# Optimization experiments

Hardware: AMD Instinct MI355X
Metric: run time of the kernel (lower is better)

## Reference

```python
import jax, jax.numpy as jnp
import numpy as np

DIM = 1024
B, TI, TJ = 8, 2048, 2048
EPS = 1e-5


def layernorm(x, g, b):
    mu = jnp.mean(x, axis=-1, keepdims=True)
    var = jnp.var(x, axis=-1, keepdims=True)
    return (x - mu) * jax.lax.rsqrt(var + EPS) * g + b


def setup_inputs() -> dict:
    key = jax.random.key(0)
    ks = jax.random.split(key, 12)
    s = 1.0 / np.sqrt(DIM)
    return {
        "target": jax.random.normal(ks[0], (B, TI, DIM), jnp.float32),
        "source_k": jax.random.normal(ks[1], (B, TJ, DIM), jnp.float32),
        "source_v": jax.random.normal(ks[2], (B, TJ, DIM), jnp.float32),
        "Wq": jax.random.uniform(ks[3], (DIM, DIM), jnp.float32, -s, s),
        "bq": jax.random.uniform(ks[4], (DIM,), jnp.float32, -s, s),
        "Wk": jax.random.uniform(ks[5], (DIM, DIM), jnp.float32, -s, s),
        "bk": jax.random.uniform(ks[6], (DIM,), jnp.float32, -s, s),
        "Wv": jax.random.uniform(ks[7], (DIM, DIM), jnp.float32, -s, s),
        "bv": jax.random.uniform(ks[8], (DIM,), jnp.float32, -s, s),
        "g_t": jnp.ones((DIM,), jnp.float32),
        "b_t": jnp.zeros((DIM,), jnp.float32),
        "g_k": jnp.ones((DIM,), jnp.float32),
        "b_k": jnp.zeros((DIM,), jnp.float32),
        "g_v": jnp.ones((DIM,), jnp.float32),
        "b_v": jnp.zeros((DIM,), jnp.float32),
    }


def reference(target, source_k, source_v, Wq, bq, Wk, bk, Wv, bv,
              g_t, b_t, g_k, b_k, g_v, b_v):
    scale = DIM ** (-0.5)
    t = layernorm(target, g_t, b_t)
    sk = layernorm(source_k, g_k, b_k)
    sv = layernorm(source_v, g_v, b_v)
    # torch Linear: x @ W.T + b
    q = jnp.einsum('bid,ed->bie', t, Wq) + bq
    k = jnp.einsum('bjd,ed->bje', sk, Wk) + bk
    v = jnp.einsum('bjd,ed->bje', sv, Wv) + bv
    dots = jnp.einsum('bid,bjd->bij', q, k) * scale
    attn = jax.nn.softmax(dots, axis=2)
    return jnp.einsum('bij,bjd->bid', attn, v)
```

## Files before the change

### kernel.cpp

```cpp
#include <hip/hip_runtime.h>
#include <cstdint>

using u16 = unsigned short;
using u32 = unsigned int;
typedef __attribute__((ext_vector_type(8))) short short8;
typedef __attribute__((ext_vector_type(4))) float f32x4;

__device__ __forceinline__ float bf2f(u16 u) { return __uint_as_float(((u32)u) << 16); }
__device__ __forceinline__ u16 f2bf(float f) {
    u32 u = __float_as_uint(f);
    u32 r = u + 0x7fffu + ((u >> 16) & 1u);
    return (u16)(r >> 16);
}

__device__ __forceinline__ void load_lds16(const void* g, void* l) {
    __builtin_amdgcn_global_load_lds((const __attribute__((address_space(1))) void*)g,
                                     (__attribute__((address_space(3))) void*)l, 16, 0, 0);
}

__device__ __forceinline__ void ln_row(const float* __restrict__ x,
                                       const float* __restrict__ gw,
                                       const float* __restrict__ bw,
                                       u16* __restrict__ y, int row) {
    const int tid = threadIdx.x;
    const float4 v = ((const float4*)(x + (size_t)row * 1024))[tid];
    float s  = v.x + v.y + v.z + v.w;
    float ss = v.x * v.x + v.y * v.y + v.z * v.z + v.w * v.w;
#pragma unroll
    for (int off = 32; off; off >>= 1) {
        s  += __shfl_xor(s, off);
        ss += __shfl_xor(ss, off);
    }
    __shared__ float sm[8];
    const int lane = tid & 63, wid = tid >> 6;
    if (lane == 0) { sm[wid] = s; sm[wid + 4] = ss; }
    __syncthreads();
    s  = sm[0] + sm[1] + sm[2] + sm[3];
    ss = sm[4] + sm[5] + sm[6] + sm[7];
    const float mu   = s * (1.0f / 1024.0f);
    const float var  = ss * (1.0f / 1024.0f) - mu * mu;
    const float rstd = rsqrtf(var + 1e-5f);
    const float4 g4 = ((const float4*)gw)[tid];
    const float4 b4 = ((const float4*)bw)[tid];
    u16 o[4];
    o[0] = f2bf((v.x - mu) * rstd * g4.x + b4.x);
    o[1] = f2bf((v.y - mu) * rstd * g4.y + b4.y);
    o[2] = f2bf((v.z - mu) * rstd * g4.z + b4.z);
    o[3] = f2bf((v.w - mu) * rstd * g4.w + b4.w);
    *(uint2*)(y + (size_t)row * 1024 + tid * 4) = *(uint2*)o;
}

__global__ __launch_bounds__(256)
void ln_cast_kernel(const float* __restrict__ x, const float* __restrict__ gw,
                    const float* __restrict__ bw, u16* __restrict__ y) {
    ln_row(x, gw, bw, y, blockIdx.x);
}

__global__ __launch_bounds__(256)
void ln3_kernel(const float* __restrict__ x0, const float* __restrict__ x1,
                const float* __restrict__ x2,
                const float* __restrict__ g0, const float* __restrict__ g1,
                const float* __restrict__ g2,
                const float* __restrict__ b0, const float* __restrict__ b1,
                const float* __restrict__ b2, u16* __restrict__ y) {
    const int bid = blockIdx.x;
    const int sel = bid >> 14;
    const int row = bid & 16383;
    const float* x  = (sel == 0) ? x0 : (sel == 1) ? x1 : x2;
    const float* gw = (sel == 0) ? g0 : (sel == 1) ? g1 : g2;
    const float* bw = (sel == 0) ? b0 : (sel == 1) ? b1 : b2;
    ln_row(x, gw, bw, y + ((size_t)sel << 24), row);
}

__global__ __launch_bounds__(256)
void cast3_kernel(const float* __restrict__ wa, const float* __restrict__ wb,
                  const float* __restrict__ wc, u16* __restrict__ oa) {
    const int bid = blockIdx.x;
    const int sel = bid >> 10;
    const float* s = (sel == 0) ? wa : (sel == 1) ? wb : wc;
    u16* d = oa + (size_t)sel * 1048576;
    const int i = (bid & 1023) * 256 + threadIdx.x;
    const float4 v = ((const float4*)s)[i];
    u16 o[4] = { f2bf(v.x), f2bf(v.y), f2bf(v.z), f2bf(v.w) };
    *(uint2*)(d + (size_t)i * 4) = *(uint2*)o;
}

template<int MODE>
__global__ __launch_bounds__(256, (MODE == 3 ? 3 : 4))
void gemm_bt(const u16* __restrict__ A, const u16* __restrict__ B,
             const float* __restrict__ bias0, const float* __restrict__ bias1,
             const float* __restrict__ bias2,
             void* __restrict__ Cout, void* __restrict__ Cout2,
             const int M, const int N, const int K, const float scale,
             const long sA, const long sB, const long sC)
{
    int bz, m0, n0;
    if (MODE == 2 || MODE == 3) {
        const int id = blockIdx.x;
        bz = id & 7;
        m0 = ((id >> 3) & 15) * 128;
        n0 = (id >> 7) * 128;
    } else {
        bz = (MODE == 4) ? blockIdx.z : 0;
        m0 = blockIdx.x * 128;
        n0 = blockIdx.y * 128;
    }
    A += (long)bz * sA;
    B += (long)bz * sB;
    const float* bias = (MODE == 4) ? (bz == 0 ? bias0 : bz == 1 ? bias1 : bias2)
                                    : bias0;
    __shared__ __align__(16) u16 As[128 * 64];
    __shared__ __align__(16) u16 Bs[128 * 64];
    const int tid  = threadIdx.x;
    const int lane = tid & 63, wid = tid >> 6;
    const int wm = (wid & 1) * 64, wn = (wid >> 1) * 64;

    const int scol = (tid & 7) ^ ((tid >> 3) & 7);
    const u16* ap = A + (long)(m0 + (tid >> 3)) * K + scol * 8;
    const u16* bp = B + (long)(n0 + (tid >> 3)) * K + scol * 8;
    u16* asd = As + wid * 512;
    u16* bsd = Bs + wid * 512;
    const long rs32 = 32L * K;

    f32x4 acc[4][4] = {};
    f32x4 acc_l[4] = {};
    const short8 ones8 = {16256, 16256, 16256, 16256, 16256, 16256, 16256, 16256};
    const int fr = lane & 15, fq = lane >> 4;
    const int sw = (fq ^ (fr & 7)) * 8;
    const int offA0 = (wm + fr) * 64 + sw;
    const int offA1 = offA0 ^ 32;
    const int offB0 = (wn + fr) * 64 + sw;
    const int offB1 = offB0 ^ 32;

    for (int k0 = 0; k0 < K; k0 += 64) {
#pragma unroll
        for (int rd = 0; rd < 4; rd++) {
            load_lds16(ap + k0 + rd * rs32, asd + rd * 2048);
            load_lds16(bp + k0 + rd * rs32, bsd + rd * 2048);
        }
        __syncthreads();
#pragma unroll
        for (int s = 0; s < 2; s++) {
            const int oa = s ? offA1 : offA0;
            const int ob = s ? offB1 : offB0;
            short8 b0 = *(const short8*)&Bs[ob];
            short8 b1 = *(const short8*)&Bs[ob + 1024];
            short8 b2 = *(const short8*)&Bs[ob + 2048];
            short8 b3 = *(const short8*)&Bs[ob + 3072];
#pragma unroll
            for (int i = 0; i < 4; i++) {
                const short8 a = *(const short8*)&As[oa + i * 1024];
                acc[i][0] = __builtin_amdgcn_mfma_f32_16x16x32_bf16(a, b0, acc[i][0], 0, 0, 0);
                acc[i][1] = __builtin_amdgcn_mfma_f32_16x16x32_bf16(a, b1, acc[i][1], 0, 0, 0);
                acc[i][2] = __builtin_amdgcn_mfma_f32_16x16x32_bf16(a, b2, acc[i][2], 0, 0, 0);
                acc[i][3] = __builtin_amdgcn_mfma_f32_16x16x32_bf16(a, b3, acc[i][3], 0, 0, 0);
                if (MODE == 3)
                    acc_l[i] = __builtin_amdgcn_mfma_f32_16x16x32_bf16(a, ones8, acc_l[i], 0, 0, 0);
            }
        }
        __syncthreads();
    }

    const int cn = lane & 15;
    const int cm = (lane >> 4) * 4;
    float invl[4][4];
    if (MODE == 3) {
#pragma unroll
        for (int i = 0; i < 4; i++)
#pragma unroll
            for (int r = 0; r < 4; r++) invl[i][r] = 1.0f / acc_l[i][r];
    }
#pragma unroll
    for (int i = 0; i < 4; i++) {
        const int gmb = m0 + wm + i * 16 + cm;
#pragma unroll
        for (int j = 0; j < 4; j++) {
            const int gn = n0 + wn + j * 16 + cn;
            const float bv = (MODE <= 1 || MODE == 4) ? bias[gn] : 0.0f;
            if (MODE == 1 || (MODE == 4 && bz == 2)) {
                u16* dst = (MODE == 4) ? (u16*)Cout2 : (u16*)Cout;
                const int batch = gmb >> 11;
                const int jj = gmb & 2047;
                u16 o[4];
#pragma unroll
                for (int r = 0; r < 4; r++) o[r] = f2bf(acc[i][j][r] + bv);
                *(uint2*)(dst + ((long)batch * N + gn) * 2048 + jj) = *(uint2*)o;
            } else if (MODE == 0 || MODE == 4) {
                u16* dst = (u16*)Cout + ((MODE == 4) ? (long)bz * 16777216 : 0);
#pragma unroll
                for (int r = 0; r < 4; r++)
                    dst[(long)(gmb + r) * N + gn] = f2bf(acc[i][j][r] + bv);
            } else {
#pragma unroll
                for (int r = 0; r < 4; r++) {
                    const long gm = gmb + r;
                    float v = acc[i][j][r];
                    if (MODE == 2) v = __expf(v * scale);
                    if (MODE == 3)
                        ((float*)Cout)[(long)bz * sC + gm * N + gn] = v * invl[i][r];
                    else
                        ((u16*)Cout)[(long)bz * sC + gm * N + gn] = f2bf(v);
                }
            }
        }
    }
}

extern "C" void kernel_launch(void* const* d_in, const int* in_sizes, int n_in,
                              void* d_out, int out_size, void* d_ws, size_t ws_size,
                              hipStream_t stream) {
    const float* target = (const float*)d_in[0];
    const float* src_k  = (const float*)d_in[1];
    const float* src_v  = (const float*)d_in[2];
    const float* Wq = (const float*)d_in[3];
    const float* bq = (const float*)d_in[4];
    const float* Wk = (const float*)d_in[5];
    const float* bk = (const float*)d_in[6];
    const float* Wv = (const float*)d_in[7];
    const float* bv = (const float*)d_in[8];
    const float* g_t = (const float*)d_in[9];
    const float* b_t = (const float*)d_in[10];
    const float* g_k = (const float*)d_in[11];
    const float* b_k = (const float*)d_in[12];
    const float* g_v = (const float*)d_in[13];
    const float* b_v = (const float*)d_in[14];

    char* ws = (char*)d_ws;
    const float scale = 0.03125f;
    const size_t MB = 1048576;

    if (ws_size >= 198 * MB) {
        u16* q   = (u16*)(ws + 0);
        u16* kk  = (u16*)(ws + 32 * MB);
        u16* vT  = (u16*)(ws + 64 * MB);
        u16* ln3 = (u16*)(ws + 96 * MB);
        u16* wqb = (u16*)(ws + 192 * MB);
        u16* S   = (u16*)(ws + 96 * MB);

        cast3_kernel<<<3072, 256, 0, stream>>>(Wq, Wk, Wv, wqb);
        ln3_kernel<<<49152, 256, 0, stream>>>(target, src_k, src_v,
                                              g_t, g_k, g_v, b_t, b_k, b_v, ln3);
        gemm_bt<4><<<dim3(128, 8, 3), 256, 0, stream>>>(ln3, wqb, bq, bk, bv,
            q, vT, 16384, 1024, 1024, 1.0f, 16777216L, 1048576L, 0);
        gemm_bt<2><<<2048, 256, 0, stream>>>(q, kk, nullptr, nullptr, nullptr, S, nullptr,
            2048, 2048, 1024, scale, 2048L * 1024, 2048L * 1024, 2048L * 2048);
        gemm_bt<3><<<1024, 256, 0, stream>>>(S, vT, nullptr, nullptr, nullptr, d_out, nullptr,
            2048, 1024, 2048, 1.0f, 2048L * 2048, 1024L * 2048, 2048L * 1024);
    } else {
        u16* q   = (u16*)(ws + 0);
        u16* kk  = (u16*)(ws + 32 * MB);
        u16* vT  = (u16*)(ws + 64 * MB);
        u16* ln  = (u16*)(ws + 96 * MB);
        u16* wqb = (u16*)(ws + 128 * MB);
        u16* wkb = wqb + 1048576;
        u16* wvb = wkb + 1048576;
        u16* S   = (u16*)(ws + 96 * MB);

        cast3_kernel<<<3072, 256, 0, stream>>>(Wq, Wk, Wv, wqb);
        ln_cast_kernel<<<16384, 256, 0, stream>>>(target, g_t, b_t, ln);
        gemm_bt<0><<<dim3(128, 8, 1), 256, 0, stream>>>(ln, wqb, bq, nullptr, nullptr,
            q, nullptr, 16384, 1024, 1024, 1.0f, 0, 0, 0);
        ln_cast_kernel<<<16384, 256, 0, stream>>>(src_k, g_k, b_k, ln);
        gemm_bt<0><<<dim3(128, 8, 1), 256, 0, stream>>>(ln, wkb, bk, nullptr, nullptr,
            kk, nullptr, 16384, 1024, 1024, 1.0f, 0, 0, 0);
        ln_cast_kernel<<<16384, 256, 0, stream>>>(src_v, g_v, b_v, ln);
        gemm_bt<1><<<dim3(128, 8, 1), 256, 0, stream>>>(ln, wvb, bv, nullptr, nullptr,
            vT, nullptr, 16384, 1024, 1024, 1.0f, 0, 0, 0);
        gemm_bt<2><<<2048, 256, 0, stream>>>(q, kk, nullptr, nullptr, nullptr, S, nullptr,
            2048, 2048, 1024, scale, 2048L * 1024, 2048L * 1024, 2048L * 2048);
        gemm_bt<3><<<1024, 256, 0, stream>>>(S, vT, nullptr, nullptr, nullptr, d_out, nullptr,
            2048, 1024, 2048, 1.0f, 2048L * 2048, 1024L * 2048, 2048L * 1024);
    }
}
```

Before: 503.7 us.

## Add 256x256 eight-wave pipelined GEMM for projection and QK stages

Adds a new 512-thread GEMM kernel with 256x256 tiles, double-buffered LDS staged through direct global-to-LDS loads, and an explicit schedule that interleaves LDS reads, async loads, barriers and MFMA groups at raised priority. It replaces the older GEMM for the fused QKV projection and the QK^T exp stage. The goal is more data reuse per tile and better overlap of memory traffic with matrix math. The cost is 128 KB of LDS and heavy register use per block, which may limit occupancy, and the hand-placed waitcnt and barrier logic is fragile.

```diff
diff --git a/kernel.cpp b/kernel.cpp
--- a/kernel.cpp
+++ b/kernel.cpp
@@ -206,6 +206,211 @@
     }
 }
 
+__device__ __forceinline__ void pbar() {
+    __builtin_amdgcn_sched_barrier(0);
+    asm volatile("" ::: "memory");
+    __builtin_amdgcn_s_barrier();
+    asm volatile("" ::: "memory");
+    __builtin_amdgcn_sched_barrier(0);
+}
+
+__device__ __forceinline__ void bar_lgkm() {
+    __builtin_amdgcn_sched_barrier(0);
+    asm volatile("s_waitcnt lgkmcnt(0)" ::: "memory");
+    __builtin_amdgcn_sched_barrier(0);
+    __builtin_amdgcn_s_barrier();
+    asm volatile("" ::: "memory");
+    __builtin_amdgcn_sched_barrier(0);
+}
+
+#define RDA4(dst, reg, off) do { \
+    dst[0] = *(const short8*)&(reg)[(off)];        \
+    dst[1] = *(const short8*)&(reg)[(off) + 1024]; \
+    dst[2] = *(const short8*)&(reg)[(off) + 2048]; \
+    dst[3] = *(const short8*)&(reg)[(off) + 3072]; } while (0)
+
+#define RDB8(dst, reg, off) do { \
+    dst[0] = *(const short8*)&(reg)[(off)];        \
+    dst[1] = *(const short8*)&(reg)[(off) + 1024]; \
+    dst[2] = *(const short8*)&(reg)[(off) + 2048]; \
+    dst[3] = *(const short8*)&(reg)[(off) + 3072]; \
+    dst[4] = *(const short8*)&(reg)[(off) + 4096]; \
+    dst[5] = *(const short8*)&(reg)[(off) + 5120]; \
+    dst[6] = *(const short8*)&(reg)[(off) + 6144]; \
+    dst[7] = *(const short8*)&(reg)[(off) + 7168]; } while (0)
+
+#define MM16(af, bf, JL) do { \
+    __builtin_amdgcn_s_setprio(1); \
+    _Pragma("unroll") \
+    for (int i_ = 0; i_ < 4; i_++) { \
+        _Pragma("unroll") \
+        for (int j_ = 0; j_ < 4; j_++) \
+            acc[i_][(JL) + j_] = __builtin_amdgcn_mfma_f32_16x16x32_bf16( \
+                af[i_], bf[(JL) + j_], acc[i_][(JL) + j_], 0, 0, 0); \
+    } \
+    __builtin_amdgcn_s_setprio(0); } while (0)
+
+#define STA(reg, hm, kt) do { \
+    const u16* s_ = apg + (hm) * rH + (long)(kt) * 64; \
+    u16* d_ = (reg) + (hm) * 8192 + w * 1024; \
+    load_lds16(s_, d_); \
+    load_lds16(s_ + rK8, d_ + 512); } while (0)
+
+#define STB(reg, hm, kt) do { \
+    const u16* s_ = bpg + (hm) * rH + (long)(kt) * 64; \
+    u16* d_ = (reg) + (hm) * 8192 + w * 1024; \
+    load_lds16(s_, d_); \
+    load_lds16(s_ + rK8, d_ + 512); } while (0)
+
+template<int MODE>
+__global__ __launch_bounds__(512, 2)
+void gemm8(const u16* __restrict__ A, const u16* __restrict__ B,
+           const float* __restrict__ bias0, const float* __restrict__ bias1,
+           const float* __restrict__ bias2,
+           void* __restrict__ Cout, void* __restrict__ Cout2,
+           const int M, const int N, const int K, const float scale,
+           const long sA, const long sB, const long sC)
+{
+    int bz, m0, n0;
+    if (MODE == 2) {
+        const int id = blockIdx.x;
+        bz = id & 7;
+        m0 = ((id >> 3) & 7) * 256;
+        n0 = (id >> 6) * 256;
+    } else {
+        bz = blockIdx.z;
+        m0 = blockIdx.x * 256;
+        n0 = blockIdx.y * 256;
+    }
+    A += (long)bz * sA;
+    B += (long)bz * sB;
+    const float* bias = (MODE == 4) ? (bz == 0 ? bias0 : bz == 1 ? bias1 : bias2)
+                                    : bias0;
+
+    __shared__ __align__(16) u16 lds[65536];
+    u16* const Ar0 = lds;
+    u16* const Ar1 = lds + 16384;
+    u16* const Br0 = lds + 32768;
+    u16* const Br1 = lds + 49152;
+
+    const int tid = threadIdx.x;
+    const int w = tid >> 6, l = tid & 63;
+    const int cgrp = (l & 7) ^ ((l >> 3) & 7);
+    const long rK8 = 8L * K;
+    const long rH  = 128L * K;
+    const u16* apg = A + (long)(m0 + w * 16 + (l >> 3)) * K + cgrp * 8;
+    const u16* bpg = B + (long)(n0 + w * 16 + (l >> 3)) * K + cgrp * 8;
+
+    const int wm = (w & 3) * 64;
+    const int wn = (w >> 2) * 128;
+    const int fr = l & 15, fq = l >> 4;
+    const int sw8 = (fq ^ (fr & 7)) * 8;
+    const int offA = (wm + fr) * 64 + sw8;
+    const int offB = (wn + fr) * 64 + sw8;
+
+    f32x4 acc[4][8] = {};
+    short8 aA0[4], aA1e[4], aA1o[4] = {};
+    short8 bB0[8], bB1[8] = {};
+
+    STA(Ar0, 0, 0); STA(Ar0, 1, 0);
+    STB(Br0, 0, 0); STB(Br0, 1, 0);
+    STA(Ar1, 0, 1); STA(Ar1, 1, 1);
+    __builtin_amdgcn_sched_barrier(0);
+    asm volatile("s_waitcnt vmcnt(4)" ::: "memory");
+    __builtin_amdgcn_s_barrier();
+    asm volatile("" ::: "memory");
+    __builtin_amdgcn_sched_barrier(0);
+
+    const int NI = K >> 7;
+    for (int it = 0; it < NI; ++it) {
+        const bool nl = (it < NI - 1);
+        const int t1 = 2 * it + 1, t2 = 2 * it + 2, t3 = 2 * it + 3;
+        RDA4(aA0, Ar0, offA);
+        STB(Br1, 0, t1);
+        bar_lgkm();
+        MM16(aA1o, bB1, 0);
+        pbar();
+        RDA4(aA1e, Ar0, offA ^ 32);
+        STB(Br1, 1, t1);
+        bar_lgkm();
+        MM16(aA1o, bB1, 4);
+        pbar();
+        RDB8(bB0, Br0, offB);
+        if (nl) STA(Ar0, 0, t2);
+        bar_lgkm();
+        MM16(aA0, bB0, 0);
+        pbar();
+        RDB8(bB1, Br0, offB ^ 32);
+        if (nl) STA(Ar0, 1, t2);
+        bar_lgkm();
+        MM16(aA0, bB0, 4);
+        __builtin_amdgcn_sched_barrier(0);
+        asm volatile("" ::: "memory");
+        if (nl) asm volatile("s_waitcnt vmcnt(4)" ::: "memory");
+        else    asm volatile("s_waitcnt vmcnt(0)" ::: "memory");
+        __builtin_amdgcn_s_barrier();
+        asm volatile("" ::: "memory");
+        __builtin_amdgcn_sched_barrier(0);
+        RDA4(aA0, Ar1, offA);
+        if (nl) STB(Br0, 0, t2);
+        bar_lgkm();
+        MM16(aA1e, bB1, 0);
+        pbar();
+        RDA4(aA1o, Ar1, offA ^ 32);
+        if (nl) STB(Br0, 1, t2);
+        bar_lgkm();
+        MM16(aA1e, bB1, 4);
+        pbar();
+        RDB8(bB0, Br1, offB);
+        if (nl) STA(Ar1, 0, t3);
+        bar_lgkm();
+        MM16(aA0, bB0, 0);
+        pbar();
+        RDB8(bB1, Br1, offB ^ 32);
+        if (nl) STA(Ar1, 1, t3);
+        bar_lgkm();
+        MM16(aA0, bB0, 4);
+        __builtin_amdgcn_sched_barrier(0);
+        asm volatile("" ::: "memory");
+        asm volatile("s_waitcnt vmcnt(4)" ::: "memory");
+        __builtin_amdgcn_s_barrier();
+        asm volatile("" ::: "memory");
+        __builtin_amdgcn_sched_barrier(0);
+    }
+    MM16(aA1o, bB1, 0);
+    MM16(aA1o, bB1, 4);
+
+    const int cn = l & 15, cm = (l >> 4) * 4;
+#pragma unroll
+    for (int i = 0; i < 4; i++) {
+        const int gmb = m0 + wm + i * 16 + cm;
+#pragma unroll
+        for (int j = 0; j < 8; j++) {
+            const int gn = n0 + wn + j * 16 + cn;
+            if (MODE == 4) {
+                const float bv = bias[gn];
+                if (bz == 2) {
+                    const int batch = gmb >> 11, jj = gmb & 2047;
+                    u16 o[4];
+#pragma unroll
+                    for (int r = 0; r < 4; r++) o[r] = f2bf(acc[i][j][r] + bv);
+                    *(uint2*)((u16*)Cout2 + ((long)batch * N + gn) * 2048 + jj) = *(uint2*)o;
+                } else {
+                    u16* dst = (u16*)Cout + (long)bz * ((long)M * N);
+#pragma unroll
+                    for (int r = 0; r < 4; r++)
+                        dst[(long)(gmb + r) * N + gn] = f2bf(acc[i][j][r] + bv);
+                }
+            } else {
+#pragma unroll
+                for (int r = 0; r < 4; r++)
+                    ((u16*)Cout)[(long)bz * sC + (long)(gmb + r) * N + gn] =
+                        f2bf(__expf(acc[i][j][r] * scale));
+            }
+        }
+    }
+}
+
 extern "C" void kernel_launch(void* const* d_in, const int* in_sizes, int n_in,
                               void* d_out, int out_size, void* d_ws, size_t ws_size,
                               hipStream_t stream) {
@@ -240,9 +445,9 @@
         cast3_kernel<<<3072, 256, 0, stream>>>(Wq, Wk, Wv, wqb);
         ln3_kernel<<<49152, 256, 0, stream>>>(target, src_k, src_v,
                                               g_t, g_k, g_v, b_t, b_k, b_v, ln3);
-        gemm_bt<4><<<dim3(128, 8, 3), 256, 0, stream>>>(ln3, wqb, bq, bk, bv,
+        gemm8<4><<<dim3(64, 4, 3), 512, 0, stream>>>(ln3, wqb, bq, bk, bv,
             q, vT, 16384, 1024, 1024, 1.0f, 16777216L, 1048576L, 0);
-        gemm_bt<2><<<2048, 256, 0, stream>>>(q, kk, nullptr, nullptr, nullptr, S, nullptr,
+        gemm8<2><<<512, 512, 0, stream>>>(q, kk, nullptr, nullptr, nullptr, S, nullptr,
             2048, 2048, 1024, scale, 2048L * 1024, 2048L * 1024, 2048L * 2048);
         gemm_bt<3><<<1024, 256, 0, stream>>>(S, vT, nullptr, nullptr, nullptr, d_out, nullptr,
             2048, 1024, 2048, 1.0f, 2048L * 2048, 1024L * 2048, 2048L * 1024);
```

New measurement: 1.152 ms. +128.7%, slower.
